# Kernel optimization log

Hardware: AMD Instinct MI355X
Metric: run time of the kernel (lower is better)

## Reference

```python
import jax, jax.numpy as jnp
import numpy as np

NUM_STATES = 16
EMBED_DIM = 512
SEQ_LEN = 512
DIRECTED = True


def setup_inputs() -> dict:
    key = jax.random.key(0)
    k1, k2, k3, k4 = jax.random.split(key, 4)
    # nn.Parameter inits: pos_initial ~ normal, pos_transition ~ orthogonal
    pos_initial = jax.random.normal(k1, (NUM_STATES, 1), dtype=jnp.float32)
    a = jax.random.normal(k2, (NUM_STATES, NUM_STATES), dtype=jnp.float32)
    q, r = jnp.linalg.qr(a)
    pos_transition = q * jnp.sign(jnp.diag(r))[None, :]  # orthogonal init
    # nn.Linear(num_states, embed_dim): W [embed_dim, num_states], bias [embed_dim]
    lim = 1.0 / np.sqrt(NUM_STATES)
    W = jax.random.uniform(k3, (EMBED_DIM, NUM_STATES), minval=-lim, maxval=lim, dtype=jnp.float32)
    b = jax.random.uniform(k4, (EMBED_DIM,), minval=-lim, maxval=lim, dtype=jnp.float32)
    return {
        "pos_initial": pos_initial,
        "pos_transition": pos_transition,
        "W": W,
        "b": b,
        "sentence_len": SEQ_LEN,
    }


def reference(pos_initial, pos_transition, W, b, sentence_len):
    n = int(sentence_len)
    k = pos_initial.shape[0]  # num_states
    ones = jnp.ones(n - 1, dtype=pos_transition.dtype)
    if DIRECTED:
        adj = jnp.diag(ones, 1)  # superdiagonal shift matrix [n, n]
    else:
        adj = jnp.diag(ones, -1) + jnp.diag(ones, 1)
    # (torch code reshapes the square adj to the same shape: a no-op)
    # kron(adj, T): [n*k, n*k]
    kron_prod = jnp.einsum('ab,cd->acbd', adj, pos_transition).reshape(n * k, n * k)
    B = jnp.eye(n * k, dtype=pos_transition.dtype) - kron_prod
    # vec_init: pos_initial column repeated per position -> [n*k]
    vec_init = jnp.tile(pos_initial[:, 0], n)
    encs = jnp.linalg.solve(B, vec_init)  # [n*k]
    stacked = encs.reshape(n, k)          # row i = states of position i
    pe = stacked @ W.T + b                # [n, embed_dim]
    return pe
```

## Files before the change

### kernel.cpp

```cpp
#include <hip/hip_runtime.h>

#define K 16
#define CH 32
#define MAXN 512

__global__ __launch_bounds__(256) void pe_stage1(
    const float* __restrict__ pos_initial,
    const float* __restrict__ pos_transition,
    float* __restrict__ stacked, int n)
{
    __shared__ float sT[K][K];
    __shared__ float sA[K][K];
    __shared__ float sB[K][K];
    __shared__ float sP[CH][K];
    __shared__ float sMp[MAXN/CH][K][K];
    __shared__ float sG[MAXN/CH][K];
    __shared__ float sU[MAXN/CH][K];
    __shared__ float sV[K];

    const int tid = threadIdx.x;
    const int r8 = tid >> 4, c8 = tid & 15;

    if (tid < K * K) sT[r8][c8] = pos_transition[tid];
    if (tid < K)     sV[tid] = pos_initial[tid];
    __syncthreads();

    if (tid < 64) {
        const int r = tid & 15;
        float trow[K];
        #pragma unroll
        for (int c = 0; c < K; ++c) trow[c] = sT[r][c];
        float s = sV[r];
        float p = s;
        if (tid < K) sP[0][r] = p;
        for (int j = 1; j < CH; ++j) {
            float sn = 0.f;
            #pragma unroll
            for (int c = 0; c < K; ++c) sn += trow[c] * __shfl(s, c);
            s = sn;
            p += s;
            if (tid < K) sP[j][r] = p;
        }
    }
    __syncthreads();

    {
        float acc;
        acc = 0.f;
        #pragma unroll
        for (int k2 = 0; k2 < K; ++k2) acc += sT[r8][k2] * sT[k2][c8];
        sA[r8][c8] = acc; __syncthreads();
        acc = 0.f;
        #pragma unroll
        for (int k2 = 0; k2 < K; ++k2) acc += sA[r8][k2] * sA[k2][c8];
        sB[r8][c8] = acc; __syncthreads();
        acc = 0.f;
        #pragma unroll
        for (int k2 = 0; k2 < K; ++k2) acc += sB[r8][k2] * sB[k2][c8];
        sA[r8][c8] = acc; __syncthreads();
        acc = 0.f;
        #pragma unroll
        for (int k2 = 0; k2 < K; ++k2) acc += sA[r8][k2] * sA[k2][c8];
        sB[r8][c8] = acc; __syncthreads();
        acc = 0.f;
        #pragma unroll
        for (int k2 = 0; k2 < K; ++k2) acc += sB[r8][k2] * sB[k2][c8];
        sA[r8][c8] = acc; __syncthreads();
    }

    const int NA = ((n - 1) >> 5) + 1;
    sMp[0][r8][c8] = (r8 == c8) ? 1.f : 0.f;
    __syncthreads();
    for (int a = 1; a < NA; ++a) {
        float acc = 0.f;
        #pragma unroll
        for (int k2 = 0; k2 < K; ++k2) acc += sMp[a-1][r8][k2] * sA[k2][c8];
        sMp[a][r8][c8] = acc;
        __syncthreads();
    }
    if (tid < NA * K) {
        const int a = r8, r = c8;
        float acc = 0.f;
        #pragma unroll
        for (int c = 0; c < K; ++c) acc += sMp[a][r][c] * sP[CH-1][c];
        sG[a][r] = acc;
    }
    __syncthreads();
    if (tid < NA * K) {
        const int a = r8, r = c8;
        float acc = 0.f;
        for (int a2 = 0; a2 < a; ++a2) acc += sG[a2][r];
        sU[a][r] = acc;
    }
    __syncthreads();

    for (int idx = tid; idx < n * K; idx += 256) {
        const int i = idx >> 4, r = idx & 15;
        const int m1 = n - 1 - i;
        const int a  = m1 >> 5, bb = m1 & (CH - 1);
        float acc = sU[a][r];
        #pragma unroll
        for (int c = 0; c < K; ++c) acc += sMp[a][r][c] * sP[bb][c];
        stacked[idx] = acc;
    }
}

__global__ __launch_bounds__(256) void pe_stage2(
    const float* __restrict__ stacked,
    const float* __restrict__ W,
    const float* __restrict__ bias,
    float* __restrict__ out, int E)
{
    __shared__ float srow[K];
    const int i = blockIdx.x;
    const int tid = threadIdx.x;
    if (tid < K) srow[tid] = stacked[i * K + tid];
    __syncthreads();
    for (int e = tid; e < E; e += 256) {
        const float4* w4 = reinterpret_cast<const float4*>(W + e * K);
        float4 w0 = w4[0], w1 = w4[1], w2 = w4[2], w3 = w4[3];
        float acc = bias[e];
        acc += w0.x * srow[0]  + w0.y * srow[1]  + w0.z * srow[2]  + w0.w * srow[3];
        acc += w1.x * srow[4]  + w1.y * srow[5]  + w1.z * srow[6]  + w1.w * srow[7];
        acc += w2.x * srow[8]  + w2.y * srow[9]  + w2.z * srow[10] + w2.w * srow[11];
        acc += w3.x * srow[12] + w3.y * srow[13] + w3.z * srow[14] + w3.w * srow[15];
        out[i * E + e] = acc;
    }
}

extern "C" void kernel_launch(void* const* d_in, const int* in_sizes, int n_in,
                              void* d_out, int out_size, void* d_ws, size_t ws_size,
                              hipStream_t stream) {
    const float* pos_initial    = (const float*)d_in[0];
    const float* pos_transition = (const float*)d_in[1];
    const float* W              = (const float*)d_in[2];
    const float* bias           = (const float*)d_in[3];
    const int E = in_sizes[3];
    const int n = out_size / E;

    float* stacked = (float*)d_ws;

    pe_stage1<<<1, 256, 0, stream>>>(pos_initial, pos_transition, stacked, n);
    pe_stage2<<<n, 256, 0, stream>>>(stacked, W, bias, (float*)d_out, E);
}
```

Before: 80.28 us.

## Fuse scan and projection into one kernel using doubling prefix recurrence

Replaces the two-kernel design (a serial single-block scan followed by a projection kernel) with one fused kernel. Every block recomputes all prefix sums through a log-depth doubling scheme that squares the transition matrix at each step, then projects its own row through W. This removes the second launch, the global workspace round trip, and the long serial chunked scan. In exchange the scan work is repeated in every one of the n blocks, adding redundant compute and shared-memory traffic per block.

```diff
diff --git a/kernel.cpp b/kernel.cpp
--- a/kernel.cpp
+++ b/kernel.cpp
@@ -1,121 +1,54 @@
 #include <hip/hip_runtime.h>
 
 #define K 16
-#define CH 32
+#define KP 17
 #define MAXN 512
 
-__global__ __launch_bounds__(256) void pe_stage1(
+__global__ __launch_bounds__(256) void pe_fused(
     const float* __restrict__ pos_initial,
     const float* __restrict__ pos_transition,
-    float* __restrict__ stacked, int n)
+    const float* __restrict__ W,
+    const float* __restrict__ bias,
+    float* __restrict__ out, int n, int E)
 {
-    __shared__ float sT[K][K];
-    __shared__ float sA[K][K];
-    __shared__ float sB[K][K];
-    __shared__ float sP[CH][K];
-    __shared__ float sMp[MAXN/CH][K][K];
-    __shared__ float sG[MAXN/CH][K];
-    __shared__ float sU[MAXN/CH][K];
-    __shared__ float sV[K];
+    __shared__ float sPow[2][K][KP];
+    __shared__ float sP[MAXN][K];
 
     const int tid = threadIdx.x;
     const int r8 = tid >> 4, c8 = tid & 15;
 
-    if (tid < K * K) sT[r8][c8] = pos_transition[tid];
-    if (tid < K)     sV[tid] = pos_initial[tid];
+    if (tid < K * K) sPow[0][r8][c8] = pos_transition[tid];
+    if (tid < K)     sP[0][tid] = pos_initial[tid];
     __syncthreads();
 
-    if (tid < 64) {
-        const int r = tid & 15;
-        float trow[K];
+    int cur = 0;
+    for (int s = 1; s < n; s <<= 1) {
+        const float (*Tm)[KP] = sPow[cur];
+
+        float sq = 0.f;
         #pragma unroll
-        for (int c = 0; c < K; ++c) trow[c] = sT[r][c];
-        float s = sV[r];
-        float p = s;
-        if (tid < K) sP[0][r] = p;
-        for (int j = 1; j < CH; ++j) {
-            float sn = 0.f;
+        for (int k2 = 0; k2 < K; ++k2) sq += Tm[r8][k2] * Tm[k2][c8];
+
+        const int jmax = (s < n - s) ? s : (n - s);
+        for (int e = tid; e < jmax * K; e += 256) {
+            const int j = e >> 4, r = e & 15;
+            float acc = sP[s - 1][r];
             #pragma unroll
-            for (int c = 0; c < K; ++c) sn += trow[c] * __shfl(s, c);
-            s = sn;
-            p += s;
-            if (tid < K) sP[j][r] = p;
+            for (int c = 0; c < K; ++c) acc += Tm[r][c] * sP[j][c];
+            sP[j + s][r] = acc;
         }
-    }
-    __syncthreads();
 
-    {
-        float acc;
-        acc = 0.f;
-        #pragma unroll
-        for (int k2 = 0; k2 < K; ++k2) acc += sT[r8][k2] * sT[k2][c8];
-        sA[r8][c8] = acc; __syncthreads();
-        acc = 0.f;
-        #pragma unroll
-        for (int k2 = 0; k2 < K; ++k2) acc += sA[r8][k2] * sA[k2][c8];
-        sB[r8][c8] = acc; __syncthreads();
-        acc = 0.f;
-        #pragma unroll
-        for (int k2 = 0; k2 < K; ++k2) acc += sB[r8][k2] * sB[k2][c8];
-        sA[r8][c8] = acc; __syncthreads();
-        acc = 0.f;
-        #pragma unroll
-        for (int k2 = 0; k2 < K; ++k2) acc += sA[r8][k2] * sA[k2][c8];
-        sB[r8][c8] = acc; __syncthreads();
-        acc = 0.f;
-        #pragma unroll
-        for (int k2 = 0; k2 < K; ++k2) acc += sB[r8][k2] * sB[k2][c8];
-        sA[r8][c8] = acc; __syncthreads();
+        sPow[cur ^ 1][r8][c8] = sq;
+        cur ^= 1;
+        __syncthreads();
     }
 
-    const int NA = ((n - 1) >> 5) + 1;
-    sMp[0][r8][c8] = (r8 == c8) ? 1.f : 0.f;
-    __syncthreads();
-    for (int a = 1; a < NA; ++a) {
-        float acc = 0.f;
-        #pragma unroll
-        for (int k2 = 0; k2 < K; ++k2) acc += sMp[a-1][r8][k2] * sA[k2][c8];
-        sMp[a][r8][c8] = acc;
-        __syncthreads();
-    }
-    if (tid < NA * K) {
-        const int a = r8, r = c8;
-        float acc = 0.f;
-        #pragma unroll
-        for (int c = 0; c < K; ++c) acc += sMp[a][r][c] * sP[CH-1][c];
-        sG[a][r] = acc;
-    }
-    __syncthreads();
-    if (tid < NA * K) {
-        const int a = r8, r = c8;
-        float acc = 0.f;
-        for (int a2 = 0; a2 < a; ++a2) acc += sG[a2][r];
-        sU[a][r] = acc;
-    }
-    __syncthreads();
+    const int i = blockIdx.x;
+    const int m1 = n - 1 - i;
+    float srow[K];
+    #pragma unroll
+    for (int r = 0; r < K; ++r) srow[r] = sP[m1][r];
 
-    for (int idx = tid; idx < n * K; idx += 256) {
-        const int i = idx >> 4, r = idx & 15;
-        const int m1 = n - 1 - i;
-        const int a  = m1 >> 5, bb = m1 & (CH - 1);
-        float acc = sU[a][r];
-        #pragma unroll
-        for (int c = 0; c < K; ++c) acc += sMp[a][r][c] * sP[bb][c];
-        stacked[idx] = acc;
-    }
-}
-
-__global__ __launch_bounds__(256) void pe_stage2(
-    const float* __restrict__ stacked,
-    const float* __restrict__ W,
-    const float* __restrict__ bias,
-    float* __restrict__ out, int E)
-{
-    __shared__ float srow[K];
-    const int i = blockIdx.x;
-    const int tid = threadIdx.x;
-    if (tid < K) srow[tid] = stacked[i * K + tid];
-    __syncthreads();
     for (int e = tid; e < E; e += 256) {
         const float4* w4 = reinterpret_cast<const float4*>(W + e * K);
         float4 w0 = w4[0], w1 = w4[1], w2 = w4[2], w3 = w4[3];
@@ -138,8 +71,6 @@
     const int E = in_sizes[3];
     const int n = out_size / E;
 
-    float* stacked = (float*)d_ws;
-
-    pe_stage1<<<1, 256, 0, stream>>>(pos_initial, pos_transition, stacked, n);
-    pe_stage2<<<n, 256, 0, stream>>>(stacked, W, bias, (float*)d_out, E);
+    pe_fused<<<n, 256, 0, stream>>>(pos_initial, pos_transition, W, bias,
+                                    (float*)d_out, n, E);
 }
```

After: 70.35 us. 1.14x faster.
